# Kernel optimization log

Hardware: AMD Instinct MI355X
Metric: run time of the kernel (lower is better)

Reference implementation:

```python
import jax, jax.numpy as jnp
import numpy as np

# Model dims (see init_kwargs / shape_source)
B = 2048      # batch
CIN = 256     # tabular input features (c_in)
NH = 512      # TabularEncoder hidden width
NENC_HID = 4  # nlayers=6 -> input layer + 4 hidden + output layer
NF = 112      # n_features = num_concepts (conv=False path)
K = 112       # num_concepts
NL = 50       # num_latent_concepts
MC = 100      # num_monte_carlo
NOUT = 200    # num_output


def setup_inputs() -> dict:
    key = jax.random.key(0)
    ks = jax.random.split(key, 8)
    x = jax.random.normal(ks[0], (B, CIN), dtype=jnp.float32)
    enc_Win = jax.random.normal(ks[1], (CIN, NH), dtype=jnp.float32) * (1.0 / np.sqrt(CIN))
    enc_bin = jnp.zeros((NH,), jnp.float32)
    enc_Wh = jax.random.normal(ks[2], (NENC_HID, NH, NH), dtype=jnp.float32) * (1.0 / np.sqrt(NH))
    enc_bh = jnp.zeros((NENC_HID, NH), jnp.float32)
    enc_Wout = jax.random.normal(ks[3], (NH, NF), dtype=jnp.float32) * (1.0 / np.sqrt(NH))
    enc_bout = jnp.zeros((NF,), jnp.float32)
    # Per-concept predictor i has first Linear of shape [NF+i, NL]; pad all to [NF+K, NL]
    # and statically slice rows [:NF+i] in the loop (unused padded rows never touched).
    pred_W1 = jax.random.normal(ks[4], (K, NF + K, NL), dtype=jnp.float32) * (1.0 / np.sqrt(NF))
    pred_b1 = jnp.zeros((K, NL), jnp.float32)
    pred_W2 = jax.random.normal(ks[5], (K, NL), dtype=jnp.float32) * (1.0 / np.sqrt(NL))
    pred_b2 = jnp.zeros((K,), jnp.float32)
    head_W = jax.random.normal(ks[6], (K, NOUT), dtype=jnp.float32) * (1.0 / np.sqrt(K))
    head_b = jnp.zeros((NOUT,), jnp.float32)
    return {
        "x": x,
        "enc_Win": enc_Win, "enc_bin": enc_bin,
        "enc_Wh": enc_Wh, "enc_bh": enc_bh,
        "enc_Wout": enc_Wout, "enc_bout": enc_bout,
        "pred_W1": pred_W1, "pred_b1": pred_b1,
        "pred_W2": pred_W2, "pred_b2": pred_b2,
        "head_W": head_W, "head_b": head_b,
        "epoch": 0,
    }


def reference(x, enc_Win, enc_bin, enc_Wh, enc_bh, enc_Wout, enc_bout,
              pred_W1, pred_b1, pred_W2, pred_b2, head_W, head_b, epoch):
    lrelu = jax.nn.leaky_relu  # negative_slope=0.01, matches nn.LeakyReLU default

    # ---- TabularEncoder (ni=CIN, nhidden=NH, nlayers=6, no=NF) ----
    h = lrelu(x @ enc_Win + enc_bin)
    for i in range(enc_Wh.shape[0]):
        h = lrelu(h @ enc_Wh[i] + enc_bh[i])
    inter = h @ enc_Wout + enc_bout                      # [B, NF]
    Bn = inter.shape[0]

    key = jax.random.key(42)
    c_hard = jnp.zeros((Bn, K, MC), inter.dtype)
    c_probs = []
    for i in range(K):
        W1 = pred_W1[i, :NF + i]                          # [NF+i, NL]
        base = inter @ W1[:NF] + pred_b1[i]               # [B, NL], shared across MC
        if i == 0:
            p1 = jax.nn.sigmoid(lrelu(base) @ pred_W2[i] + pred_b2[i])   # [B]
            p = jnp.broadcast_to(p1[:, None], (Bn, MC))   # expand(-1,-1,MC)
        else:
            # add contribution of the i previously sampled hard concepts, per MC sample
            hpre = base[:, None, :] + jnp.einsum('bim,ih->bmh', c_hard[:, :i], W1[NF:])  # [B,MC,NL]
            p = jax.nn.sigmoid(jnp.einsum('bmh,h->bm', lrelu(hpre), pred_W2[i]) + pred_b2[i])  # [B,MC]
        key, sk = jax.random.split(key)
        samp = jax.random.bernoulli(sk, p).astype(p.dtype)  # torch.bernoulli(concept)
        c_hard = c_hard.at[:, i, :].set(samp)
        c_probs.append(p)

    c_prob = jnp.stack(c_probs, axis=1)                   # [B, K, MC]

    # ---- Head: MC average of softmax probabilities (pred_dim > 1 branch) ----
    logits = jnp.einsum('bkm,ko->bmo', c_hard, head_W) + head_b   # [B, MC, NOUT]
    probs = jax.nn.softmax(logits, axis=-1).mean(axis=1)          # [B, NOUT]
    y_pred_logits = jnp.log(probs + 1e-6)
    return (c_prob, y_pred_logits, c_hard)
```

## Files before the change

### kernel.cpp

```cpp
#include <hip/hip_runtime.h>

typedef unsigned int u32;
typedef unsigned short u16;
typedef unsigned long long u64;

#define YOFF  22937600ull
#define CHOFF 23347200ull

#define OFF_HA    0ull
#define OFF_HB    4194304ull
#define OFF_INTER 8388608ull

__host__ __device__ inline u32 rotl32_(u32 x, int r) { return (x << r) | (x >> (32 - r)); }
__host__ __device__ inline void tf2x32(u32 k0, u32 k1, u32 c0, u32 c1, u32& o0, u32& o1) {
  u32 ks0 = k0, ks1 = k1, ks2 = k0 ^ k1 ^ 0x1BD11BDAu;
  u32 x0 = c0 + ks0, x1 = c1 + ks1;
  const int RA[4] = {13, 15, 26, 6}, RB[4] = {17, 29, 16, 24};
  for (int i = 0; i < 5; ++i) {
    const int* R = (i & 1) ? RB : RA;
    for (int j = 0; j < 4; ++j) { x0 += x1; x1 = rotl32_(x1, R[j]); x1 ^= x0; }
    switch (i) {
      case 0: x0 += ks1; x1 += ks2 + 1u; break;
      case 1: x0 += ks2; x1 += ks0 + 2u; break;
      case 2: x0 += ks0; x1 += ks1 + 3u; break;
      case 3: x0 += ks1; x1 += ks2 + 4u; break;
      case 4: x0 += ks2; x1 += ks0 + 5u; break;
    }
  }
  o0 = x0; o1 = x1;
}

struct SKeys { u32 v[224]; };

template <bool DO_LRELU>
__global__ __launch_bounds__(256) void gemm_bias(const float* __restrict__ A,
                                                 const float* __restrict__ Bm,
                                                 const float* __restrict__ bias,
                                                 float* __restrict__ C,
                                                 int M, int N, int K) {
  __shared__ float As[32][65];
  __shared__ float Bs[32][65];
  const int bm = blockIdx.y * 64, bn = blockIdx.x * 64;
  const int t = threadIdx.x;
  const int ty = t >> 4, tx = t & 15;
  float acc[4][4] = {};
  for (int k0 = 0; k0 < K; k0 += 32) {
#pragma unroll
    for (int l = 0; l < 2; ++l) {
      int e = l * 256 + t;
      int m = e >> 3, k4 = e & 7;
      float4 v = *(const float4*)(A + (size_t)(bm + m) * K + (k0 + k4 * 4));
      As[k4 * 4 + 0][m] = v.x; As[k4 * 4 + 1][m] = v.y;
      As[k4 * 4 + 2][m] = v.z; As[k4 * 4 + 3][m] = v.w;
    }
#pragma unroll
    for (int l = 0; l < 2; ++l) {
      int e = l * 256 + t;
      int k = e >> 4, n4 = e & 15;
      int gn = bn + n4 * 4;
      if (gn < N) {
        float4 v = *(const float4*)(Bm + (size_t)(k0 + k) * N + gn);
        Bs[k][n4 * 4 + 0] = v.x; Bs[k][n4 * 4 + 1] = v.y;
        Bs[k][n4 * 4 + 2] = v.z; Bs[k][n4 * 4 + 3] = v.w;
      } else {
        Bs[k][n4 * 4 + 0] = 0.f; Bs[k][n4 * 4 + 1] = 0.f;
        Bs[k][n4 * 4 + 2] = 0.f; Bs[k][n4 * 4 + 3] = 0.f;
      }
    }
    __syncthreads();
#pragma unroll
    for (int kk = 0; kk < 32; ++kk) {
      float a[4], b[4];
#pragma unroll
      for (int j = 0; j < 4; ++j) { a[j] = As[kk][ty * 4 + j]; b[j] = Bs[kk][tx * 4 + j]; }
#pragma unroll
      for (int i = 0; i < 4; ++i)
#pragma unroll
        for (int j = 0; j < 4; ++j) acc[i][j] = fmaf(a[i], b[j], acc[i][j]);
    }
    __syncthreads();
  }
#pragma unroll
  for (int i = 0; i < 4; ++i) {
#pragma unroll
    for (int j = 0; j < 4; ++j) {
      int m = bm + ty * 4 + i, n = bn + tx * 4 + j;
      if (n < N) {
        float s = acc[i][j] + bias[n];
        if (DO_LRELU) { if (s < 0.f) s = 0.01f * s; }
        C[(size_t)m * N + n] = s;
      }
    }
  }
}

__global__ __launch_bounds__(256) void base_kernel(const float* __restrict__ inter,
                                                   const float* __restrict__ W1,
                                                   const float* __restrict__ pb1,
                                                   float* __restrict__ out) {
  __shared__ float As[112][65];
  __shared__ float Ws[112][64];
  const int i = blockIdx.y;
  const int b0 = blockIdx.x * 64;
  const int t = threadIdx.x;
  const int ty = t >> 4, tx = t & 15;
#pragma unroll
  for (int l = 0; l < 7; ++l) {
    int e4 = l * 256 + t;
    int k4 = e4 % 28, bs = e4 / 28;
    float4 v = *(const float4*)(inter + (size_t)(b0 + bs) * 112 + k4 * 4);
    As[k4 * 4 + 0][bs] = v.x; As[k4 * 4 + 1][bs] = v.y;
    As[k4 * 4 + 2][bs] = v.z; As[k4 * 4 + 3][bs] = v.w;
  }
#pragma unroll
  for (int l = 0; l < 28; ++l) {
    int e = l * 256 + t;
    int r = e >> 6, c = e & 63;
    Ws[r][c] = (c < 50) ? W1[(size_t)i * 11200 + r * 50 + c] : 0.f;
  }
  __syncthreads();
  float acc[4][4] = {};
  for (int kk = 0; kk < 112; ++kk) {
    float a[4], b[4];
#pragma unroll
    for (int j = 0; j < 4; ++j) { a[j] = As[kk][ty * 4 + j]; b[j] = Ws[kk][tx * 4 + j]; }
#pragma unroll
    for (int ii = 0; ii < 4; ++ii)
#pragma unroll
      for (int j = 0; j < 4; ++j) acc[ii][j] = fmaf(a[ii], b[j], acc[ii][j]);
  }
#pragma unroll
  for (int ii = 0; ii < 4; ++ii) {
#pragma unroll
    for (int j = 0; j < 4; ++j) {
      int b = b0 + ty * 4 + ii, h = tx * 4 + j;
      if (h < 50) {
        out[CHOFF + (size_t)b * 11200 + (size_t)i * 100 + h] = acc[ii][j] + pb1[i * 50 + h];
      }
    }
  }
}

__global__ __launch_bounds__(512) void sample_kernel(const float* __restrict__ W1,
                                                     const float* __restrict__ W2,
                                                     const float* __restrict__ b2,
                                                     float* __restrict__ out, SKeys sks) {
  const int t = threadIdx.x;
  const int p = blockIdx.x * 500 + t;
  const bool active = (t < 500) && (p < 204800);
  const int b = p / 100;
  const int m = p - b * 100;
  const size_t rowbase = (size_t)b * 11200 + m;
  const float* __restrict__ baserow = out + CHOFF + (size_t)b * 11200;
  u64 lo = 0, hi = 0;

  if (active) {
    for (int i = 0; i < 112; ++i) {
      const float* __restrict__ Wi = W1 + (size_t)i * 11200 + 5600;
      float acc[50];
#pragma unroll
      for (int h = 0; h < 50; ++h) acc[h] = 0.f;
      for (int r = 0; r < i; ++r) {
        float c = (((r < 64) ? (lo >> r) : (hi >> (r - 64))) & 1ull) ? 1.f : 0.f;
        const float* __restrict__ wr = Wi + r * 50;
#pragma unroll
        for (int h = 0; h < 50; ++h) acc[h] = fmaf(c, wr[h], acc[h]);
      }
      const float* __restrict__ w2 = W2 + i * 50;
      const float* bs = baserow + (size_t)i * 100;
      float s = 0.f;
#pragma unroll
      for (int h = 0; h < 50; ++h) {
        float v = acc[h] + bs[h];
        if (v < 0.f) v = 0.01f * v;
        s = fmaf(v, w2[h], s);
      }
      float l = s + b2[i];
      float pr = 1.f / (1.f + expf(-l));
      u32 a0, a1;
      tf2x32(sks.v[2 * i], sks.v[2 * i + 1], 0u, (u32)p, a0, a1);
      u32 fb = ((a0 ^ a1) >> 9) | 0x3F800000u;
      float u; __builtin_memcpy(&u, &fb, 4); u -= 1.f;
      int smp = (u < pr) ? 1 : 0;
      out[rowbase + (size_t)i * 100] = pr;
      if (smp) { if (i < 64) lo |= 1ull << i; else hi |= 1ull << (i - 64); }
    }
    for (int i = 0; i < 112; ++i) {
      u64 bit = (i < 64) ? (lo >> i) : (hi >> (i - 64));
      out[CHOFF + rowbase + (size_t)i * 100] = (bit & 1ull) ? 1.0f : 0.0f;
    }
  }
}

__global__ __launch_bounds__(256) void head_kernel(const float* __restrict__ HW,
                                                   const float* __restrict__ hb,
                                                   float* __restrict__ out) {
  __shared__ unsigned char cS[100][116];
  __shared__ float lgS[50][201];
  const int b = blockIdx.x;
  const int t = threadIdx.x;
  for (int e = t; e < 11200; e += 256) {
    int k = e / 100, m = e - k * 100;
    cS[m][k] = (out[CHOFF + (size_t)b * 11200 + (size_t)k * 100 + m] != 0.f) ? 1 : 0;
  }
  __syncthreads();
  float pacc = 0.f;
  for (int mh = 0; mh < 2; ++mh) {
    for (int l = 0; l < 3; ++l) {
      int tile = l * 256 + t;
      if (tile < 625) {
        int o0 = (tile % 25) * 8;
        int m0 = (tile / 25) * 2;
        float acc[2][8] = {};
        for (int k = 0; k < 112; ++k) {
          float4 wa = *(const float4*)(HW + (size_t)k * 200 + o0);
          float4 wb = *(const float4*)(HW + (size_t)k * 200 + o0 + 4);
          float w[8] = {wa.x, wa.y, wa.z, wa.w, wb.x, wb.y, wb.z, wb.w};
          float c0 = (float)cS[mh * 50 + m0][k];
          float c1 = (float)cS[mh * 50 + m0 + 1][k];
#pragma unroll
          for (int jo = 0; jo < 8; ++jo) {
            acc[0][jo] = fmaf(c0, w[jo], acc[0][jo]);
            acc[1][jo] = fmaf(c1, w[jo], acc[1][jo]);
          }
        }
#pragma unroll
        for (int im = 0; im < 2; ++im)
#pragma unroll
          for (int jo = 0; jo < 8; ++jo) {
            int o = o0 + jo;
            lgS[m0 + im][o] = acc[im][jo] + hb[o];
          }
      }
    }
    __syncthreads();
    if (t < 50) {
      int m = t;
      float mx = -3.0e38f;
      for (int o = 0; o < 200; ++o) mx = fmaxf(mx, lgS[m][o]);
      float s = 0.f;
      for (int o = 0; o < 200; ++o) {
        float e = expf(lgS[m][o] - mx);
        lgS[m][o] = e; s += e;
      }
      float inv = 1.f / s;
      for (int o = 0; o < 200; ++o) lgS[m][o] = lgS[m][o] * inv;
    }
    __syncthreads();
    if (t < 200) { for (int m = 0; m < 50; ++m) pacc += lgS[m][t]; }
    __syncthreads();
  }
  if (t < 200) {
    out[YOFF + (size_t)b * 200 + t] = logf(pacc / 100.f + 1e-6f);
  }
}

extern "C" void kernel_launch(void* const* d_in, const int* in_sizes, int n_in,
                              void* d_out, int out_size, void* d_ws, size_t ws_size,
                              hipStream_t stream) {
  const float* x    = (const float*)d_in[0];
  const float* Win  = (const float*)d_in[1];
  const float* bin  = (const float*)d_in[2];
  const float* Wh   = (const float*)d_in[3];
  const float* bh   = (const float*)d_in[4];
  const float* Wout = (const float*)d_in[5];
  const float* bout = (const float*)d_in[6];
  const float* pW1  = (const float*)d_in[7];
  const float* pb1  = (const float*)d_in[8];
  const float* pW2  = (const float*)d_in[9];
  const float* pb2  = (const float*)d_in[10];
  const float* hW   = (const float*)d_in[11];
  const float* hb   = (const float*)d_in[12];
  float* out = (float*)d_out;
  char* ws = (char*)d_ws;

  float* hA     = (float*)(ws + OFF_HA);
  float* hB     = (float*)(ws + OFF_HB);
  float* interB = (float*)(ws + OFF_INTER);

  gemm_bias<true ><<<dim3(8, 32), 256, 0, stream>>>(x,  Win,             bin,          hA,     2048, 512, 256);
  gemm_bias<true ><<<dim3(8, 32), 256, 0, stream>>>(hA, Wh + 0 * 262144, bh + 0 * 512, hB,     2048, 512, 512);
  gemm_bias<true ><<<dim3(8, 32), 256, 0, stream>>>(hB, Wh + 1 * 262144, bh + 1 * 512, hA,     2048, 512, 512);
  gemm_bias<true ><<<dim3(8, 32), 256, 0, stream>>>(hA, Wh + 2 * 262144, bh + 2 * 512, hB,     2048, 512, 512);
  gemm_bias<true ><<<dim3(8, 32), 256, 0, stream>>>(hB, Wh + 3 * 262144, bh + 3 * 512, hA,     2048, 512, 512);
  gemm_bias<false><<<dim3(2, 32), 256, 0, stream>>>(hA, Wout,            bout,         interB, 2048, 112, 512);

  base_kernel<<<dim3(32, 112), 256, 0, stream>>>(interB, pW1, pb1, out);

  SKeys sks;
  {
    u32 k0 = 0u, k1 = 42u;
    for (int i = 0; i < 112; ++i) {
      u32 nk0, nk1, s0, s1;
      tf2x32(k0, k1, 0u, 0u, nk0, nk1);
      tf2x32(k0, k1, 0u, 1u, s0, s1);
      sks.v[2 * i] = s0; sks.v[2 * i + 1] = s1;
      k0 = nk0; k1 = nk1;
    }
  }
  sample_kernel<<<410, 512, 0, stream>>>(pW1, pW2, pb2, out, sks);

  head_kernel<<<2048, 256, 0, stream>>>(hW, hb, out);
}
```

Measured before the change: 3.718 ms.

## Double-buffer weight rows with vector loads in sampler and split hard-concept expansion

Rewrites the sequential sampling kernel to load each 50-wide W1 row as float4/float2 vectors into two alternating register buffers, so the next row's load overlaps the current row's FMAs. The base row is also vector-loaded and folded into the tail. Per-thread sample bitmasks go to a workspace buffer, and a separate expand kernel writes c_hard with coalesced stores instead of strided per-thread writes. An opaque zero from inline asm keeps the compiler from hoisting loads, and launch bounds ask for 3 waves per SIMD, which adds register pressure risk plus one extra launch.

```diff
diff --git a/kernel.cpp b/kernel.cpp
--- a/kernel.cpp
+++ b/kernel.cpp
@@ -141,54 +141,142 @@
   }
 }
 
-__global__ __launch_bounds__(512) void sample_kernel(const float* __restrict__ W1,
-                                                     const float* __restrict__ W2,
-                                                     const float* __restrict__ b2,
-                                                     float* __restrict__ out, SKeys sks) {
+
+struct Row50 { float4 q[12]; float2 e; };
+
+#define LOADROW_E(R, ptr) do {                                              \
+  const float* _p = (ptr);                                                  \
+  _Pragma("unroll")                                                         \
+  for (int _j = 0; _j < 12; ++_j) (R).q[_j] = *(const float4*)(_p + 4 * _j);\
+  (R).e = *(const float2*)(_p + 48);                                        \
+} while (0)
+
+#define LOADROW_O(R, ptr) do {                                              \
+  const float* _p = (ptr);                                                  \
+  (R).e = *(const float2*)_p;                                               \
+  _Pragma("unroll")                                                         \
+  for (int _j = 0; _j < 12; ++_j) (R).q[_j] = *(const float4*)(_p + 2 + 4 * _j);\
+} while (0)
+
+#define FMAROW_E(R, c) do {                                                 \
+  float _c = (c);                                                           \
+  _Pragma("unroll")                                                         \
+  for (int _j = 0; _j < 12; ++_j) {                                         \
+    acc[4 * _j + 0] = fmaf(_c, (R).q[_j].x, acc[4 * _j + 0]);               \
+    acc[4 * _j + 1] = fmaf(_c, (R).q[_j].y, acc[4 * _j + 1]);               \
+    acc[4 * _j + 2] = fmaf(_c, (R).q[_j].z, acc[4 * _j + 2]);               \
+    acc[4 * _j + 3] = fmaf(_c, (R).q[_j].w, acc[4 * _j + 3]);               \
+  }                                                                         \
+  acc[48] = fmaf(_c, (R).e.x, acc[48]);                                     \
+  acc[49] = fmaf(_c, (R).e.y, acc[49]);                                     \
+} while (0)
+
+#define FMAROW_O(R, c) do {                                                 \
+  float _c = (c);                                                           \
+  acc[0] = fmaf(_c, (R).e.x, acc[0]);                                       \
+  acc[1] = fmaf(_c, (R).e.y, acc[1]);                                       \
+  _Pragma("unroll")                                                         \
+  for (int _j = 0; _j < 12; ++_j) {                                         \
+    acc[2 + 4 * _j + 0] = fmaf(_c, (R).q[_j].x, acc[2 + 4 * _j + 0]);       \
+    acc[2 + 4 * _j + 1] = fmaf(_c, (R).q[_j].y, acc[2 + 4 * _j + 1]);       \
+    acc[2 + 4 * _j + 2] = fmaf(_c, (R).q[_j].z, acc[2 + 4 * _j + 2]);       \
+    acc[2 + 4 * _j + 3] = fmaf(_c, (R).q[_j].w, acc[2 + 4 * _j + 3]);       \
+  }                                                                         \
+} while (0)
+
+#define CBIT(r) (((((r) < 64 ? lo : hi) >> ((r) & 63)) & 1ull) ? 1.f : 0.f)
+
+#define TAIL(R) do {                                                        \
+  const float* __restrict__ w2 = W2 + i * 50;             \
+  float s = 0.f;                                                            \
+  _Pragma("unroll")                                                         \
+  for (int _j = 0; _j < 12; ++_j) {                                         \
+    float _v;                                                               \
+    _v = acc[4 * _j + 0] + (R).q[_j].x; if (_v < 0.f) _v = 0.01f * _v; s = fmaf(_v, w2[4 * _j + 0], s); \
+    _v = acc[4 * _j + 1] + (R).q[_j].y; if (_v < 0.f) _v = 0.01f * _v; s = fmaf(_v, w2[4 * _j + 1], s); \
+    _v = acc[4 * _j + 2] + (R).q[_j].z; if (_v < 0.f) _v = 0.01f * _v; s = fmaf(_v, w2[4 * _j + 2], s); \
+    _v = acc[4 * _j + 3] + (R).q[_j].w; if (_v < 0.f) _v = 0.01f * _v; s = fmaf(_v, w2[4 * _j + 3], s); \
+  }                                                                         \
+  { float _v = acc[48] + (R).e.x; if (_v < 0.f) _v = 0.01f * _v; s = fmaf(_v, w2[48], s); } \
+  { float _v = acc[49] + (R).e.y; if (_v < 0.f) _v = 0.01f * _v; s = fmaf(_v, w2[49], s); } \
+  float l = s + b2v[i];                                                     \
+  float pr = 1.f / (1.f + expf(-l));                                        \
+  u32 a0, a1;                                                               \
+  tf2x32(sks.v[2 * i], sks.v[2 * i + 1], 0u, (u32)p, a0, a1);               \
+  u32 fb = ((a0 ^ a1) >> 9) | 0x3F800000u;                                  \
+  float uu; __builtin_memcpy(&uu, &fb, 4); uu -= 1.f;                       \
+  u64 sbit = (uu < pr) ? 1ull : 0ull;                                       \
+  out[(size_t)b * 11200 + (size_t)i * 100 + m] = pr;    \
+  if (i < 64) lo |= sbit << i; else hi |= sbit << (i - 64);                 \
+} while (0)
+
+__global__ __launch_bounds__(512, 3) void sample_kernel5(const float* __restrict__ W1,
+                                                         const float* __restrict__ W2,
+                                                         const float* __restrict__ b2v,
+                                                         float* __restrict__ out,
+                                                         u32* __restrict__ masks, SKeys sks) {
   const int t = threadIdx.x;
   const int p = blockIdx.x * 500 + t;
-  const bool active = (t < 500) && (p < 204800);
+  if (t >= 500 || p >= 204800) return;
   const int b = p / 100;
   const int m = p - b * 100;
-  const size_t rowbase = (size_t)b * 11200 + m;
   const float* __restrict__ baserow = out + CHOFF + (size_t)b * 11200;
+  int vz;
+  asm volatile("v_mov_b32 %0, 0" : "=v"(vz));
   u64 lo = 0, hi = 0;
-
-  if (active) {
-    for (int i = 0; i < 112; ++i) {
-      const float* __restrict__ Wi = W1 + (size_t)i * 11200 + 5600;
-      float acc[50];
-#pragma unroll
-      for (int h = 0; h < 50; ++h) acc[h] = 0.f;
-      for (int r = 0; r < i; ++r) {
-        float c = (((r < 64) ? (lo >> r) : (hi >> (r - 64))) & 1ull) ? 1.f : 0.f;
-        const float* __restrict__ wr = Wi + r * 50;
-#pragma unroll
-        for (int h = 0; h < 50; ++h) acc[h] = fmaf(c, wr[h], acc[h]);
-      }
-      const float* __restrict__ w2 = W2 + i * 50;
-      const float* bs = baserow + (size_t)i * 100;
-      float s = 0.f;
-#pragma unroll
-      for (int h = 0; h < 50; ++h) {
-        float v = acc[h] + bs[h];
-        if (v < 0.f) v = 0.01f * v;
-        s = fmaf(v, w2[h], s);
-      }
-      float l = s + b2[i];
-      float pr = 1.f / (1.f + expf(-l));
-      u32 a0, a1;
-      tf2x32(sks.v[2 * i], sks.v[2 * i + 1], 0u, (u32)p, a0, a1);
-      u32 fb = ((a0 ^ a1) >> 9) | 0x3F800000u;
-      float u; __builtin_memcpy(&u, &fb, 4); u -= 1.f;
-      int smp = (u < pr) ? 1 : 0;
-      out[rowbase + (size_t)i * 100] = pr;
-      if (smp) { if (i < 64) lo |= 1ull << i; else hi |= 1ull << (i - 64); }
-    }
-    for (int i = 0; i < 112; ++i) {
-      u64 bit = (i < 64) ? (lo >> i) : (hi >> (i - 64));
-      out[CHOFF + rowbase + (size_t)i * 100] = (bit & 1ull) ? 1.0f : 0.0f;
-    }
+  float acc[50];
+  Row50 A, B;
+
+#pragma unroll 1
+  for (int i = 0; i < 112; ++i) {
+#pragma unroll
+    for (int h = 0; h < 50; ++h) acc[h] = 0.f;
+    const float* __restrict__ Wi = W1 + (size_t)i * 11200 + 5600 + vz;
+    const float* __restrict__ bs = baserow + (size_t)i * 100 + vz;
+    if (i == 0) {
+      LOADROW_E(A, bs);
+      TAIL(A);
+    } else {
+      LOADROW_E(A, Wi);
+      int r = 0;
+      for (; r + 2 < i; r += 2) {
+        LOADROW_O(B, Wi + (r + 1) * 50);
+        FMAROW_E(A, CBIT(r));
+        LOADROW_E(A, Wi + (r + 2) * 50);
+        FMAROW_O(B, CBIT(r + 1));
+      }
+      if (r + 1 < i) {
+        LOADROW_O(B, Wi + (r + 1) * 50);
+        FMAROW_E(A, CBIT(r));
+        LOADROW_E(A, bs);
+        FMAROW_O(B, CBIT(r + 1));
+        TAIL(A);
+      } else {
+        LOADROW_E(B, bs);
+        FMAROW_E(A, CBIT(r));
+        TAIL(B);
+      }
+    }
+  }
+  u32* mp = masks + (size_t)p * 4;
+  mp[0] = (u32)lo; mp[1] = (u32)(lo >> 32);
+  mp[2] = (u32)hi; mp[3] = (u32)(hi >> 32);
+}
+
+__global__ __launch_bounds__(256) void expand_kernel(const u32* __restrict__ masks,
+                                                     float* __restrict__ out) {
+  __shared__ u32 mW[100][4];
+  const int b = blockIdx.x;
+  const int t = threadIdx.x;
+  if (t < 100) {
+    const u32* mp = masks + ((size_t)b * 100 + t) * 4;
+    mW[t][0] = mp[0]; mW[t][1] = mp[1]; mW[t][2] = mp[2]; mW[t][3] = mp[3];
+  }
+  __syncthreads();
+  for (int e = t; e < 11200; e += 256) {
+    int i = e / 100, m = e - i * 100;
+    u32 word = mW[m][i >> 5];
+    out[CHOFF + (size_t)b * 11200 + e] = (float)((word >> (i & 31)) & 1u);
   }
 }
 
@@ -277,6 +365,7 @@
   float* hA     = (float*)(ws + OFF_HA);
   float* hB     = (float*)(ws + OFF_HB);
   float* interB = (float*)(ws + OFF_INTER);
+  u32*   masks  = (u32*)(ws + OFF_HB);
 
   gemm_bias<true ><<<dim3(8, 32), 256, 0, stream>>>(x,  Win,             bin,          hA,     2048, 512, 256);
   gemm_bias<true ><<<dim3(8, 32), 256, 0, stream>>>(hA, Wh + 0 * 262144, bh + 0 * 512, hB,     2048, 512, 512);
@@ -298,7 +387,8 @@
       k0 = nk0; k1 = nk1;
     }
   }
-  sample_kernel<<<410, 512, 0, stream>>>(pW1, pW2, pb2, out, sks);
+  sample_kernel5<<<410, 512, 0, stream>>>(pW1, pW2, pb2, out, masks, sks);
+  expand_kernel<<<2048, 256, 0, stream>>>(masks, out);
 
   head_kernel<<<2048, 256, 0, stream>>>(hW, hb, out);
 }
```

After: 9.878 ms. 2.66x slower.

## Split sampling hidden dim across two waves and shrink GEMM M-tile

Applied to the files above, without the earlier changes.

The sequential Bernoulli sampling kernel now gives each (batch, MC) sample to two wavefronts, each holding 25 of the 50 hidden units. Partial activations are exchanged through shared memory to form the dot product. This halves the per-thread register footprint and launches many more small blocks, aiming to raise occupancy in what is likely the dominant kernel. Sampled bits are written as compact masks and expanded by a separate kernel, which replaces the strided per-thread stores. The encoder GEMM tile shrinks to 32 rows to double the block count, at the cost of duplicate work across the waves and two extra barriers per concept.

```diff
diff --git a/kernel.cpp b/kernel.cpp
--- a/kernel.cpp
+++ b/kernel.cpp
@@ -38,16 +38,15 @@
                                                  const float* __restrict__ bias,
                                                  float* __restrict__ C,
                                                  int M, int N, int K) {
-  __shared__ float As[32][65];
+  __shared__ float As[32][33];
   __shared__ float Bs[32][65];
-  const int bm = blockIdx.y * 64, bn = blockIdx.x * 64;
+  const int bm = blockIdx.y * 32, bn = blockIdx.x * 64;
   const int t = threadIdx.x;
   const int ty = t >> 4, tx = t & 15;
-  float acc[4][4] = {};
+  float acc[2][4] = {};
   for (int k0 = 0; k0 < K; k0 += 32) {
-#pragma unroll
-    for (int l = 0; l < 2; ++l) {
-      int e = l * 256 + t;
+    {
+      int e = t;
       int m = e >> 3, k4 = e & 7;
       float4 v = *(const float4*)(A + (size_t)(bm + m) * K + (k0 + k4 * 4));
       As[k4 * 4 + 0][m] = v.x; As[k4 * 4 + 1][m] = v.y;
@@ -70,21 +69,23 @@
     __syncthreads();
 #pragma unroll
     for (int kk = 0; kk < 32; ++kk) {
-      float a[4], b[4];
-#pragma unroll
-      for (int j = 0; j < 4; ++j) { a[j] = As[kk][ty * 4 + j]; b[j] = Bs[kk][tx * 4 + j]; }
-#pragma unroll
-      for (int i = 0; i < 4; ++i)
+      float a[2], b[4];
+#pragma unroll
+      for (int j = 0; j < 2; ++j) a[j] = As[kk][ty * 2 + j];
+#pragma unroll
+      for (int j = 0; j < 4; ++j) b[j] = Bs[kk][tx * 4 + j];
+#pragma unroll
+      for (int i = 0; i < 2; ++i)
 #pragma unroll
         for (int j = 0; j < 4; ++j) acc[i][j] = fmaf(a[i], b[j], acc[i][j]);
     }
     __syncthreads();
   }
 #pragma unroll
-  for (int i = 0; i < 4; ++i) {
+  for (int i = 0; i < 2; ++i) {
 #pragma unroll
     for (int j = 0; j < 4; ++j) {
-      int m = bm + ty * 4 + i, n = bn + tx * 4 + j;
+      int m = bm + ty * 2 + i, n = bn + tx * 4 + j;
       if (n < N) {
         float s = acc[i][j] + bias[n];
         if (DO_LRELU) { if (s < 0.f) s = 0.01f * s; }
@@ -141,54 +142,102 @@
   }
 }
 
-__global__ __launch_bounds__(512) void sample_kernel(const float* __restrict__ W1,
-                                                     const float* __restrict__ W2,
-                                                     const float* __restrict__ b2,
-                                                     float* __restrict__ out, SKeys sks) {
-  const int t = threadIdx.x;
-  const int p = blockIdx.x * 500 + t;
-  const bool active = (t < 500) && (p < 204800);
+__global__ __launch_bounds__(128, 4) void sample_team(const float* __restrict__ W1,
+                                                      const float* __restrict__ W2,
+                                                      const float* __restrict__ b2v,
+                                                      float* __restrict__ out,
+                                                      u32* __restrict__ masks, SKeys sks) {
+  __shared__ float vbuf[2][64][28];
+  const int t = threadIdx.x;
+  const int lane = t & 63;
+  const int subu = __builtin_amdgcn_readfirstlane(t >> 6);
+  const int p = blockIdx.x * 64 + lane;
   const int b = p / 100;
   const int m = p - b * 100;
-  const size_t rowbase = (size_t)b * 11200 + m;
-  const float* __restrict__ baserow = out + CHOFF + (size_t)b * 11200;
+  const float* __restrict__ baserow = out + CHOFF + (size_t)b * 11200 + subu * 25;
   u64 lo = 0, hi = 0;
-
-  if (active) {
-    for (int i = 0; i < 112; ++i) {
-      const float* __restrict__ Wi = W1 + (size_t)i * 11200 + 5600;
-      float acc[50];
-#pragma unroll
-      for (int h = 0; h < 50; ++h) acc[h] = 0.f;
-      for (int r = 0; r < i; ++r) {
-        float c = (((r < 64) ? (lo >> r) : (hi >> (r - 64))) & 1ull) ? 1.f : 0.f;
-        const float* __restrict__ wr = Wi + r * 50;
-#pragma unroll
-        for (int h = 0; h < 50; ++h) acc[h] = fmaf(c, wr[h], acc[h]);
-      }
-      const float* __restrict__ w2 = W2 + i * 50;
+  float acc[25], pv[25];
+
+  for (int i = 0; i < 112; ++i) {
+#pragma unroll
+    for (int h = 0; h < 25; ++h) acc[h] = 0.f;
+    {
+      const float* __restrict__ Wi = W1 + (size_t)i * 11200 + 5600 + subu * 25;
+      int r = 0;
+      for (; r + 1 < i; r += 2) {
+        float cA = (((r < 64) ? (lo >> r) : (hi >> (r - 64))) & 1ull) ? 1.f : 0.f;
+        int r2 = r + 1;
+        float cB = (((r2 < 64) ? (lo >> r2) : (hi >> (r2 - 64))) & 1ull) ? 1.f : 0.f;
+        const float* __restrict__ wA = Wi + (size_t)r * 50;
+#pragma unroll
+        for (int h = 0; h < 25; ++h)
+          acc[h] = fmaf(cB, wA[50 + h], fmaf(cA, wA[h], acc[h]));
+      }
+      if (r < i) {
+        float cA = (((r < 64) ? (lo >> r) : (hi >> (r - 64))) & 1ull) ? 1.f : 0.f;
+        const float* __restrict__ wA = Wi + (size_t)r * 50;
+#pragma unroll
+        for (int h = 0; h < 25; ++h) acc[h] = fmaf(cA, wA[h], acc[h]);
+      }
+    }
+    {
       const float* bs = baserow + (size_t)i * 100;
-      float s = 0.f;
-#pragma unroll
-      for (int h = 0; h < 50; ++h) {
-        float v = acc[h] + bs[h];
-        if (v < 0.f) v = 0.01f * v;
-        s = fmaf(v, w2[h], s);
-      }
-      float l = s + b2[i];
-      float pr = 1.f / (1.f + expf(-l));
-      u32 a0, a1;
-      tf2x32(sks.v[2 * i], sks.v[2 * i + 1], 0u, (u32)p, a0, a1);
-      u32 fb = ((a0 ^ a1) >> 9) | 0x3F800000u;
-      float u; __builtin_memcpy(&u, &fb, 4); u -= 1.f;
-      int smp = (u < pr) ? 1 : 0;
-      out[rowbase + (size_t)i * 100] = pr;
-      if (smp) { if (i < 64) lo |= 1ull << i; else hi |= 1ull << (i - 64); }
-    }
-    for (int i = 0; i < 112; ++i) {
-      u64 bit = (i < 64) ? (lo >> i) : (hi >> (i - 64));
-      out[CHOFF + rowbase + (size_t)i * 100] = (bit & 1ull) ? 1.0f : 0.0f;
-    }
+#pragma unroll
+      for (int h = 0; h < 25; ++h) {
+        float x = acc[h] + bs[h];
+        acc[h] = (x < 0.f) ? 0.01f * x : x;
+      }
+    }
+#pragma unroll
+    for (int h = 0; h < 25; ++h) vbuf[subu][lane][h] = acc[h];
+    __syncthreads();
+#pragma unroll
+    for (int h = 0; h < 25; ++h) pv[h] = vbuf[1 - subu][lane][h];
+    __syncthreads();
+    const float* __restrict__ w2 = W2 + i * 50;
+    float s = 0.f;
+    if (subu == 0) {
+#pragma unroll
+      for (int h = 0; h < 25; ++h) s = fmaf(acc[h], w2[h], s);
+#pragma unroll
+      for (int h = 0; h < 25; ++h) s = fmaf(pv[h], w2[25 + h], s);
+    } else {
+#pragma unroll
+      for (int h = 0; h < 25; ++h) s = fmaf(pv[h], w2[h], s);
+#pragma unroll
+      for (int h = 0; h < 25; ++h) s = fmaf(acc[h], w2[25 + h], s);
+    }
+    float l = s + b2v[i];
+    float pr = 1.f / (1.f + expf(-l));
+    u32 a0, a1;
+    tf2x32(sks.v[2 * i], sks.v[2 * i + 1], 0u, (u32)p, a0, a1);
+    u32 fb = ((a0 ^ a1) >> 9) | 0x3F800000u;
+    float uu; __builtin_memcpy(&uu, &fb, 4); uu -= 1.f;
+    u64 sbit = (uu < pr) ? 1ull : 0ull;
+    if (subu == 0) out[(size_t)b * 11200 + (size_t)i * 100 + m] = pr;
+    if (i < 64) lo |= sbit << i; else hi |= sbit << (i - 64);
+  }
+  if (subu == 0) {
+    u32* mp = masks + (size_t)p * 4;
+    mp[0] = (u32)lo; mp[1] = (u32)(lo >> 32);
+    mp[2] = (u32)hi; mp[3] = (u32)(hi >> 32);
+  }
+}
+
+__global__ __launch_bounds__(256) void expand_kernel(const u32* __restrict__ masks,
+                                                     float* __restrict__ out) {
+  __shared__ u32 mW[100][4];
+  const int b = blockIdx.x;
+  const int t = threadIdx.x;
+  if (t < 100) {
+    const u32* mp = masks + ((size_t)b * 100 + t) * 4;
+    mW[t][0] = mp[0]; mW[t][1] = mp[1]; mW[t][2] = mp[2]; mW[t][3] = mp[3];
+  }
+  __syncthreads();
+  for (int e = t; e < 11200; e += 256) {
+    int i = e / 100, m = e - i * 100;
+    u32 word = mW[m][i >> 5];
+    out[CHOFF + (size_t)b * 11200 + e] = (float)((word >> (i & 31)) & 1u);
   }
 }
 
@@ -277,13 +326,14 @@
   float* hA     = (float*)(ws + OFF_HA);
   float* hB     = (float*)(ws + OFF_HB);
   float* interB = (float*)(ws + OFF_INTER);
-
-  gemm_bias<true ><<<dim3(8, 32), 256, 0, stream>>>(x,  Win,             bin,          hA,     2048, 512, 256);
-  gemm_bias<true ><<<dim3(8, 32), 256, 0, stream>>>(hA, Wh + 0 * 262144, bh + 0 * 512, hB,     2048, 512, 512);
-  gemm_bias<true ><<<dim3(8, 32), 256, 0, stream>>>(hB, Wh + 1 * 262144, bh + 1 * 512, hA,     2048, 512, 512);
-  gemm_bias<true ><<<dim3(8, 32), 256, 0, stream>>>(hA, Wh + 2 * 262144, bh + 2 * 512, hB,     2048, 512, 512);
-  gemm_bias<true ><<<dim3(8, 32), 256, 0, stream>>>(hB, Wh + 3 * 262144, bh + 3 * 512, hA,     2048, 512, 512);
-  gemm_bias<false><<<dim3(2, 32), 256, 0, stream>>>(hA, Wout,            bout,         interB, 2048, 112, 512);
+  u32*   masks  = (u32*)(ws + OFF_HB);
+
+  gemm_bias<true ><<<dim3(8, 64), 256, 0, stream>>>(x,  Win,             bin,          hA,     2048, 512, 256);
+  gemm_bias<true ><<<dim3(8, 64), 256, 0, stream>>>(hA, Wh + 0 * 262144, bh + 0 * 512, hB,     2048, 512, 512);
+  gemm_bias<true ><<<dim3(8, 64), 256, 0, stream>>>(hB, Wh + 1 * 262144, bh + 1 * 512, hA,     2048, 512, 512);
+  gemm_bias<true ><<<dim3(8, 64), 256, 0, stream>>>(hA, Wh + 2 * 262144, bh + 2 * 512, hB,     2048, 512, 512);
+  gemm_bias<true ><<<dim3(8, 64), 256, 0, stream>>>(hB, Wh + 3 * 262144, bh + 3 * 512, hA,     2048, 512, 512);
+  gemm_bias<false><<<dim3(2, 64), 256, 0, stream>>>(hA, Wout,            bout,         interB, 2048, 112, 512);
 
   base_kernel<<<dim3(32, 112), 256, 0, stream>>>(interB, pW1, pb1, out);
 
@@ -298,7 +348,8 @@
       k0 = nk0; k1 = nk1;
     }
   }
-  sample_kernel<<<410, 512, 0, stream>>>(pW1, pW2, pb2, out, sks);
+  sample_team<<<3200, 128, 0, stream>>>(pW1, pW2, pb2, out, masks, sks);
+  expand_kernel<<<2048, 256, 0, stream>>>(masks, out);
 
   head_kernel<<<2048, 256, 0, stream>>>(hW, hb, out);
 }
```

Result: slower. 3.822 ms (+2.8%).
